# Kernel tuning notes

Hardware: AMD Instinct MI355X
Metric: run time of the kernel (lower is better)

## Reference

```python
import jax, jax.numpy as jnp
import numpy as np

B, S, E, H, NE, K = 4, 1024, 1024, 16, 8, 2
DFF = 4 * E
DH = E // H
EPS = 1e-5


def _ln(x, g, b):
    m = jnp.mean(x, axis=-1, keepdims=True)
    v = jnp.mean(jnp.square(x - m), axis=-1, keepdims=True)
    return (x - m) * jax.lax.rsqrt(v + EPS) * g + b


def setup_inputs() -> dict:
    key = jax.random.key(0)
    ks = jax.random.split(key, 20)
    n = lambda k, sh, s: (jax.random.normal(k, sh, jnp.float32) * s)
    return {
        'x': n(ks[0], (B, S, E), 1.0),
        'ln1_g': jnp.ones((E,), jnp.float32), 'ln1_b': jnp.zeros((E,), jnp.float32),
        'wq': n(ks[1], (E, E), 0.02), 'bq': jnp.zeros((E,), jnp.float32),
        'wk': n(ks[2], (E, E), 0.02), 'bk': jnp.zeros((E,), jnp.float32),
        'wv': n(ks[3], (E, E), 0.02), 'bv': jnp.zeros((E,), jnp.float32),
        'wo': n(ks[4], (E, E), 0.02), 'bo': jnp.zeros((E,), jnp.float32),
        'ln2_g': jnp.ones((E,), jnp.float32), 'ln2_b': jnp.zeros((E,), jnp.float32),
        'sw1': n(ks[5], (E, DFF), 0.02), 'sb1': jnp.zeros((DFF,), jnp.float32),
        'sw2': n(ks[6], (DFF, E), 0.02), 'sb2': jnp.zeros((E,), jnp.float32),
        'ew1': n(ks[7], (NE, E, DFF), 0.02), 'eb1': jnp.zeros((NE, DFF), jnp.float32),
        'ew2': n(ks[8], (NE, DFF, E), 0.02), 'eb2': jnp.zeros((NE, E), jnp.float32),
        'w_gate': n(ks[9], (E, NE), 1.0),
    }


def reference(x, ln1_g, ln1_b, wq, bq, wk, bk, wv, bv, wo, bo,
              ln2_g, ln2_b, sw1, sb1, sw2, sb2, ew1, eb1, ew2, eb2, w_gate):
    # --- self-attention sublayer (eval: no dropout) ---
    res1 = x
    h = _ln(x, ln1_g, ln1_b)
    q = (h @ wq + bq).reshape(B, S, H, DH)
    k = (h @ wk + bk).reshape(B, S, H, DH)
    v = (h @ wv + bv).reshape(B, S, H, DH)
    scores = jnp.einsum('bqhd,bkhd->bhqk', q, k) / jnp.sqrt(jnp.float32(DH))
    attn = jax.nn.softmax(scores, axis=-1)
    ctx = jnp.einsum('bhqk,bkhd->bqhd', attn, v).reshape(B, S, E)
    x = res1 + (ctx @ wo + bo)

    # --- MoE sublayer ---
    res2 = x
    h2 = _ln(x, ln2_g, ln2_b)
    shared = jax.nn.gelu(h2 @ sw1 + sb1, approximate=False) @ sw2 + sb2

    # router (eval: clean logits, no noise)
    logits = h2 @ w_gate                                  # (B,S,NE)
    top_vals, top_idx = jax.lax.top_k(logits, K)          # (B,S,K)
    top_gates = jax.nn.softmax(top_vals, axis=-1)
    onehot = jax.nn.one_hot(top_idx, NE, dtype=x.dtype)   # (B,S,K,NE)
    gates = jnp.einsum('bsk,bske->bse', top_gates, onehot)
    probs = jax.nn.softmax(logits, axis=-1).reshape(-1, NE)
    P = probs.mean(0)
    f = (gates > 0).astype(x.dtype).reshape(-1, NE).mean(0)
    aux_loss = NE * jnp.sum(P * f)

    # dense all-expert compute, gated combine (matches original math)
    eh = jax.nn.gelu(jnp.einsum('bse,neh->bnsh', h2, ew1) + eb1[None, :, None, :],
                     approximate=False)
    eo = jnp.einsum('bnsh,nhe->bnse', eh, ew2) + eb2[None, :, None, :]
    expert_out = jnp.einsum('bnse,bsn->bse', eo, gates)

    return res2 + shared + expert_out, aux_loss
```

## Files before the change

### kernel.cpp

```cpp
#include <hip/hip_runtime.h>
#include <stdint.h>

#define B_    4
#define S_    1024
#define E_    1024
#define H_    16
#define NE_   8
#define DFF_  4096
#define NT_   4096
#define QS_   3072
#define ROWCAP9_ 13440

typedef unsigned short u16;
typedef short bf16x8 __attribute__((ext_vector_type(8)));
typedef float f32x4 __attribute__((ext_vector_type(4)));

__device__ __forceinline__ float bf2f(u16 u){ unsigned v = ((unsigned)u) << 16; return __builtin_bit_cast(float, v); }
__device__ __forceinline__ u16 f2bf(float f){ unsigned x = __builtin_bit_cast(unsigned, f); return (u16)((x + 0x7FFFu + ((x >> 16) & 1u)) >> 16); }
__device__ __forceinline__ float gelu_f(float x){ return 0.5f * x * (1.f + erff(x * 0.70710678118f)); }

__device__ __forceinline__ void gl_lds16(const u16* g, u16* l){
  __builtin_amdgcn_global_load_lds((__attribute__((address_space(1))) void*)(const_cast<u16*>(g)),
                                   (__attribute__((address_space(3))) void*)(l), 16, 0, 0);
}

#define KSW32(l)   ((((l) & 3) ^ (((l) >> 3) & 3)) << 3)
#define FRAGOFF(l) (((l) & 15) * 32 + (((((l) >> 4) ^ (((l) >> 1) & 3))) << 3))

#define VMCNT(n)   asm volatile("s_waitcnt vmcnt(" #n ")" ::: "memory")

__launch_bounds__(256)
__global__ void ln_kernel(const float* __restrict__ x, const float* __restrict__ g,
                          const float* __restrict__ be, u16* __restrict__ out)
{
  const int row = blockIdx.x;
  const float4 v = ((const float4*)(x + (size_t)row * E_))[threadIdx.x];
  float s = v.x + v.y + v.z + v.w;
  #pragma unroll
  for(int mm = 32; mm >= 1; mm >>= 1) s += __shfl_xor(s, mm);
  __shared__ float red[8];
  const int wid = threadIdx.x >> 6;
  if((threadIdx.x & 63) == 0) red[wid] = s;
  __syncthreads();
  const float mean = (red[0] + red[1] + red[2] + red[3]) * (1.0f / E_);
  const float d0 = v.x - mean, d1 = v.y - mean, d2 = v.z - mean, d3 = v.w - mean;
  float q2 = d0*d0 + d1*d1 + d2*d2 + d3*d3;
  #pragma unroll
  for(int mm = 32; mm >= 1; mm >>= 1) q2 += __shfl_xor(q2, mm);
  if((threadIdx.x & 63) == 0) red[4 + wid] = q2;
  __syncthreads();
  const float var = (red[4] + red[5] + red[6] + red[7]) * (1.0f / E_);
  const float rs = rsqrtf(var + 1e-5f);
  const float4 gg = ((const float4*)g)[threadIdx.x];
  const float4 bb = ((const float4*)be)[threadIdx.x];
  ushort4 o;
  o.x = f2bf(d0 * rs * gg.x + bb.x);
  o.y = f2bf(d1 * rs * gg.y + bb.y);
  o.z = f2bf(d2 * rs * gg.z + bb.z);
  o.w = f2bf(d3 * rs * gg.w + bb.w);
  ((ushort4*)(out + (size_t)row * E_))[threadIdx.x] = o;
}

__launch_bounds__(256)
__global__ void ln_router_kernel(const float* __restrict__ x, const float* __restrict__ g,
                                 const float* __restrict__ be, u16* __restrict__ out,
                                 const float* __restrict__ wg,
                                 float* __restrict__ probs, float* __restrict__ tkgate,
                                 int* __restrict__ tkidx, int* __restrict__ counts)
{
  const int row = blockIdx.x;
  const int tid = threadIdx.x, lane = tid & 63, wid = tid >> 6;
  const float4 v = ((const float4*)(x + (size_t)row * E_))[tid];
  float s = v.x + v.y + v.z + v.w;
  #pragma unroll
  for(int mm = 32; mm >= 1; mm >>= 1) s += __shfl_xor(s, mm);
  __shared__ float red[8];
  __shared__ float part[4][8];
  if(lane == 0) red[wid] = s;
  __syncthreads();
  const float mean = (red[0] + red[1] + red[2] + red[3]) * (1.0f / E_);
  const float d0 = v.x - mean, d1 = v.y - mean, d2 = v.z - mean, d3 = v.w - mean;
  float q2 = d0*d0 + d1*d1 + d2*d2 + d3*d3;
  #pragma unroll
  for(int mm = 32; mm >= 1; mm >>= 1) q2 += __shfl_xor(q2, mm);
  if(lane == 0) red[4 + wid] = q2;
  __syncthreads();
  const float var = (red[4] + red[5] + red[6] + red[7]) * (1.0f / E_);
  const float rs = rsqrtf(var + 1e-5f);
  const float4 gg = ((const float4*)g)[tid];
  const float4 bb = ((const float4*)be)[tid];
  ushort4 o;
  o.x = f2bf(d0 * rs * gg.x + bb.x);
  o.y = f2bf(d1 * rs * gg.y + bb.y);
  o.z = f2bf(d2 * rs * gg.z + bb.z);
  o.w = f2bf(d3 * rs * gg.w + bb.w);
  ((ushort4*)(out + (size_t)row * E_))[tid] = o;
  const float h0 = bf2f(o.x), h1 = bf2f(o.y), h2v = bf2f(o.z), h3 = bf2f(o.w);
  float a[8];
  #pragma unroll
  for(int e = 0; e < 8; e++) a[e] = 0.f;
  const float* wr = wg + (size_t)(tid * 4) * NE_;
  #pragma unroll
  for(int j = 0; j < 4; j++){
    const float hj = (j == 0) ? h0 : (j == 1) ? h1 : (j == 2) ? h2v : h3;
    const float4 w0 = *(const float4*)(wr + j * NE_);
    const float4 w1 = *(const float4*)(wr + j * NE_ + 4);
    a[0] += hj * w0.x; a[1] += hj * w0.y; a[2] += hj * w0.z; a[3] += hj * w0.w;
    a[4] += hj * w1.x; a[5] += hj * w1.y; a[6] += hj * w1.z; a[7] += hj * w1.w;
  }
  #pragma unroll
  for(int mm = 1; mm < 64; mm <<= 1)
    #pragma unroll
    for(int e = 0; e < 8; e++) a[e] += __shfl_xor(a[e], mm);
  if(lane == 0)
    #pragma unroll
    for(int e = 0; e < 8; e++) part[wid][e] = a[e];
  __syncthreads();
  if(tid == 0){
    float lg[8];
    #pragma unroll
    for(int e = 0; e < 8; e++) lg[e] = part[0][e] + part[1][e] + part[2][e] + part[3][e];
    float mx = lg[0];
    #pragma unroll
    for(int e = 1; e < 8; e++) mx = fmaxf(mx, lg[e]);
    float se = 0.f, ex[8];
    #pragma unroll
    for(int e = 0; e < 8; e++){ ex[e] = expf(lg[e] - mx); se += ex[e]; }
    const float inv = 1.f / se;
    float* pr = probs + (size_t)row * 8;
    #pragma unroll
    for(int e = 0; e < 8; e++) pr[e] = ex[e] * inv;
    int i1 = 0; float v1 = lg[0];
    #pragma unroll
    for(int e = 1; e < 8; e++) if(lg[e] > v1){ v1 = lg[e]; i1 = e; }
    int i2 = -1; float v2 = -3.4e38f;
    #pragma unroll
    for(int e = 0; e < 8; e++) if(e != i1 && lg[e] > v2){ v2 = lg[e]; i2 = e; }
    const float t = expf(v2 - v1);
    tkidx[row*2] = i1; tkidx[row*2+1] = i2;
    tkgate[row*2] = 1.f / (1.f + t); tkgate[row*2+1] = t / (1.f + t);
    atomicAdd(&counts[i1], 1); atomicAdd(&counts[i2], 1);
  }
}

__device__ __forceinline__ void transpose_body(const float* __restrict__ W, u16* __restrict__ WT, int K, int N)
{
  __shared__ __align__(16) u16 t[64][72];
  const int k0 = blockIdx.x * 64, n0 = blockIdx.y * 64;
  const int tid = threadIdx.x;
  const int kr = tid >> 2;
  const int nc = (tid & 3) * 4;
  #pragma unroll
  for(int p = 0; p < 4; p++){
    float4 v = *(const float4*)(W + (size_t)(k0 + kr) * N + n0 + nc + p * 16);
    t[nc + p*16 + 0][kr] = f2bf(v.x);
    t[nc + p*16 + 1][kr] = f2bf(v.y);
    t[nc + p*16 + 2][kr] = f2bf(v.z);
    t[nc + p*16 + 3][kr] = f2bf(v.w);
  }
  __syncthreads();
  const int nr = tid >> 3;
  const int kg = (tid & 7) * 8;
  #pragma unroll
  for(int p = 0; p < 2; p++){
    const int nn = nr + p * 32;
    unsigned u0 = t[nn][kg+0], u1 = t[nn][kg+1], u2 = t[nn][kg+2], u3 = t[nn][kg+3];
    unsigned u4 = t[nn][kg+4], u5 = t[nn][kg+5], u6 = t[nn][kg+6], u7 = t[nn][kg+7];
    uint4 o;
    o.x = u0 | (u1 << 16); o.y = u2 | (u3 << 16); o.z = u4 | (u5 << 16); o.w = u6 | (u7 << 16);
    *(uint4*)(WT + (size_t)(n0 + nn) * K + k0 + kg) = o;
  }
}

__launch_bounds__(256)
__global__ void transpose_kernel(const float* __restrict__ W, u16* __restrict__ WT, int K, int N)
{ transpose_body(W, WT, K, N); }

__launch_bounds__(256)
__global__ void transpose4_kernel(const float* wq, const float* wk, const float* wv, const float* wo,
                                  u16* __restrict__ WT)
{
  const float* W = (blockIdx.z == 0) ? wq : (blockIdx.z == 1) ? wk : (blockIdx.z == 2) ? wv : wo;
  transpose_body(W, WT + (size_t)blockIdx.z * E_ * E_, E_, E_);
}

__launch_bounds__(256)
__global__ void transpose9_kernel(const float* __restrict__ ew, const float* __restrict__ sw,
                                  u16* __restrict__ WT, int K, int N)
{
  const float* W = (blockIdx.z < 8) ? (ew + (size_t)blockIdx.z * K * N) : sw;
  transpose_body(W, WT + (size_t)blockIdx.z * K * N, K, N);
}

__global__ void prep_kernel(const float* __restrict__ bq, const float* __restrict__ bk,
                            const float* __restrict__ bv, float* __restrict__ bcat,
                            int* __restrict__ counts, int* __restrict__ rowlist,
                            const float* __restrict__ eb1, const float* __restrict__ sb1,
                            float* __restrict__ b9up,
                            const float* __restrict__ eb2, const float* __restrict__ sb2,
                            float* __restrict__ b9dn)
{
  const int stride = gridDim.x * 256;
  for(int i = blockIdx.x * 256 + threadIdx.x; i < 9 * DFF_; i += stride){
    b9up[i] = (i < 8 * DFF_) ? eb1[i] : sb1[i - 8 * DFF_];
    if(i < 9 * E_)   b9dn[i] = (i < 8 * E_) ? eb2[i] : sb2[i - 8 * E_];
    if(i < QS_)      bcat[i] = (i < E_) ? bq[i] : (i < 2*E_) ? bk[i - E_] : bv[i - 2*E_];
    if(i < 16)       counts[i] = 0;
    if(i < ROWCAP9_) rowlist[i] = -1;
  }
}

__launch_bounds__(256)
__global__ void route_kernel(const int* __restrict__ counts, const int* __restrict__ tkidx,
                             const float* __restrict__ tkgate, const float* __restrict__ probs,
                             int* __restrict__ aoff, int* __restrict__ rowlist,
                             float* __restrict__ rowgate, float* __restrict__ outaux, int addShared)
{
  __shared__ int cur[8];
  __shared__ int aoffs[10];
  __shared__ float part[4][8];
  const int tid = threadIdx.x, lane = tid & 63, wid = tid >> 6;
  if(tid == 0){
    int o = 0;
    for(int e = 0; e < 8; e++){ aoffs[e] = o; cur[e] = o; o += ((counts[e] + 127) >> 7) << 7; }
    aoffs[8] = o; aoffs[9] = o + (addShared ? NT_ : 0);
    for(int e = 0; e < 10; e++) aoff[e] = aoffs[e];
  }
  __syncthreads();
  for(int t = tid; t < NT_; t += 256){
    #pragma unroll
    for(int kk = 0; kk < 2; kk++){
      const int e = tkidx[t*2 + kk];
      const int pos = atomicAdd(&cur[e], 1);
      rowlist[pos] = t; rowgate[pos] = tkgate[t*2 + kk];
    }
    if(addShared){ rowlist[aoffs[8] + t] = t; rowgate[aoffs[8] + t] = 1.f; }
  }
  float a[8];
  #pragma unroll
  for(int e = 0; e < 8; e++) a[e] = 0.f;
  for(int t = tid; t < NT_; t += 256){
    const float* p = probs + (size_t)t * 8;
    #pragma unroll
    for(int e = 0; e < 8; e++) a[e] += p[e];
  }
  #pragma unroll
  for(int mm = 1; mm < 64; mm <<= 1)
    #pragma unroll
    for(int e = 0; e < 8; e++) a[e] += __shfl_xor(a[e], mm);
  if(lane == 0)
    #pragma unroll
    for(int e = 0; e < 8; e++) part[wid][e] = a[e];
  __syncthreads();
  if(tid == 0){
    float aux = 0.f;
    for(int e = 0; e < 8; e++){
      const float P = (part[0][e] + part[1][e] + part[2][e] + part[3][e]) / (float)NT_;
      const float f = (float)counts[e] / (float)NT_;
      aux += P * f;
    }
    outaux[0] = (float)NE_ * aux;
  }
}

template<int MODE>
__launch_bounds__(256)
__global__ void gemm_kernel(const u16* __restrict__ A, const u16* __restrict__ Bt,
                            int N, int Kd, const float* __restrict__ bias,
                            u16* __restrict__ outB)
{
  __shared__ __align__(16) u16 As0[4096], Bs0[4096], As1[4096], Bs1[4096];
  const int tid = threadIdx.x, lane = tid & 63, wid = tid >> 6;
  const int wm = wid >> 1, wn = wid & 1;
  const int tm = blockIdx.y * 128, tn = blockIdx.x * 128;

  const f32x4 zero = {0.f, 0.f, 0.f, 0.f};
  f32x4 acc[4][4];
  #pragma unroll
  for(int m = 0; m < 4; m++)
    #pragma unroll
    for(int n = 0; n < 4; n++) acc[m][n] = zero;

  const int ksw = KSW32(lane);
  const u16* gA0 = A  + (size_t)(tm + wid*32 + (lane >> 2)) * Kd + ksw;
  const u16* gA1 = gA0 + (size_t)16 * Kd;
  const u16* gB0 = Bt + (size_t)(tn + wid*32 + (lane >> 2)) * Kd + ksw;
  const u16* gB1 = gB0 + (size_t)16 * Kd;
  u16* lA0 = As0 + wid*1024; u16* lA1 = lA0 + 512;
  u16* lB0 = Bs0 + wid*1024; u16* lB1 = lB0 + 512;
  u16* lA0b = As1 + wid*1024; u16* lA1b = lA0b + 512;
  u16* lB0b = Bs1 + wid*1024; u16* lB1b = lB0b + 512;
  const int fo = FRAGOFF(lane);
  const int fA = wm * 2048, fB = wn * 2048;

  for(int k0 = 0; k0 < Kd; k0 += 64){
    __syncthreads();
    gl_lds16(gA0 + k0, lA0);  gl_lds16(gA1 + k0, lA1);
    gl_lds16(gB0 + k0, lB0);  gl_lds16(gB1 + k0, lB1);
    gl_lds16(gA0 + k0+32, lA0b); gl_lds16(gA1 + k0+32, lA1b);
    gl_lds16(gB0 + k0+32, lB0b); gl_lds16(gB1 + k0+32, lB1b);
    __syncthreads();
    bf16x8 aF[4], bF[4];
    #pragma unroll
    for(int m = 0; m < 4; m++) aF[m] = *(const bf16x8*)(As0 + fA + m*512 + fo);
    #pragma unroll
    for(int n = 0; n < 4; n++) bF[n] = *(const bf16x8*)(Bs0 + fB + n*512 + fo);
    #pragma unroll
    for(int m = 0; m < 4; m++)
      #pragma unroll
      for(int n = 0; n < 4; n++)
        acc[m][n] = __builtin_amdgcn_mfma_f32_16x16x32_bf16(aF[m], bF[n], acc[m][n], 0, 0, 0);
    #pragma unroll
    for(int m = 0; m < 4; m++) aF[m] = *(const bf16x8*)(As1 + fA + m*512 + fo);
    #pragma unroll
    for(int n = 0; n < 4; n++) bF[n] = *(const bf16x8*)(Bs1 + fB + n*512 + fo);
    #pragma unroll
    for(int m = 0; m < 4; m++)
      #pragma unroll
      for(int n = 0; n < 4; n++)
        acc[m][n] = __builtin_amdgcn_mfma_f32_16x16x32_bf16(aF[m], bF[n], acc[m][n], 0, 0, 0);
  }

  #pragma unroll
  for(int m = 0; m < 4; m++){
    const int row = tm + wm*64 + m*16 + ((lane >> 4) << 2);
    #pragma unroll
    for(int n = 0; n < 4; n++){
      const int col = tn + wn*64 + n*16 + (lane & 15);
      const float bc = bias[col];
      #pragma unroll
      for(int r = 0; r < 4; r++){
        const float v = acc[m][n][r] + bc;
        const size_t idx = (size_t)(row + r) * N + col;
        if constexpr(MODE == 0) outB[idx] = f2bf(v);
        else outB[idx] = f2bf(gelu_f(v));
      }
    }
  }
}

template<int MODE>
__launch_bounds__(256)
__global__ void gemm64_kernel(const u16* __restrict__ A, const u16* __restrict__ Bt,
                              int N, int Kd, const float* __restrict__ bias,
                              float* __restrict__ outF, const float* __restrict__ resid)
{
  __shared__ __align__(16) u16 As0[2048], As1[2048], Bs0[4096], Bs1[4096];
  const int tid = threadIdx.x, lane = tid & 63, wid = tid >> 6;
  const int wm = wid >> 1, wn = wid & 1;
  const int tm = blockIdx.y * 64, tn = blockIdx.x * 128;

  const f32x4 zero = {0.f, 0.f, 0.f, 0.f};
  f32x4 acc[2][4];
  #pragma unroll
  for(int m = 0; m < 2; m++)
    #pragma unroll
    for(int n = 0; n < 4; n++) acc[m][n] = zero;

  const int ksw = KSW32(lane);
  const u16* gA = A + (size_t)(tm + wid*16 + (lane >> 2)) * Kd + ksw;
  const u16* gB0 = Bt + (size_t)(tn + wid*32 + (lane >> 2)) * Kd + ksw;
  const u16* gB1 = gB0 + (size_t)16 * Kd;
  u16* lA  = As0 + wid*512;  u16* lAb = As1 + wid*512;
  u16* lB0 = Bs0 + wid*1024; u16* lB1 = lB0 + 512;
  u16* lB0b = Bs1 + wid*1024; u16* lB1b = lB0b + 512;
  const int fo = FRAGOFF(lane);
  const int fA = wm * 1024, fB = wn * 2048;

  for(int k0 = 0; k0 < Kd; k0 += 64){
    __syncthreads();
    gl_lds16(gA + k0, lA);
    gl_lds16(gB0 + k0, lB0); gl_lds16(gB1 + k0, lB1);
    gl_lds16(gA + k0+32, lAb);
    gl_lds16(gB0 + k0+32, lB0b); gl_lds16(gB1 + k0+32, lB1b);
    __syncthreads();
    bf16x8 aF[2], bF[4];
    #pragma unroll
    for(int m = 0; m < 2; m++) aF[m] = *(const bf16x8*)(As0 + fA + m*512 + fo);
    #pragma unroll
    for(int n = 0; n < 4; n++) bF[n] = *(const bf16x8*)(Bs0 + fB + n*512 + fo);
    #pragma unroll
    for(int m = 0; m < 2; m++)
      #pragma unroll
      for(int n = 0; n < 4; n++)
        acc[m][n] = __builtin_amdgcn_mfma_f32_16x16x32_bf16(aF[m], bF[n], acc[m][n], 0, 0, 0);
    #pragma unroll
    for(int m = 0; m < 2; m++) aF[m] = *(const bf16x8*)(As1 + fA + m*512 + fo);
    #pragma unroll
    for(int n = 0; n < 4; n++) bF[n] = *(const bf16x8*)(Bs1 + fB + n*512 + fo);
    #pragma unroll
    for(int m = 0; m < 2; m++)
      #pragma unroll
      for(int n = 0; n < 4; n++)
        acc[m][n] = __builtin_amdgcn_mfma_f32_16x16x32_bf16(aF[m], bF[n], acc[m][n], 0, 0, 0);
  }

  #pragma unroll
  for(int m = 0; m < 2; m++){
    const int row = tm + wm*32 + m*16 + ((lane >> 4) << 2);
    #pragma unroll
    for(int n = 0; n < 4; n++){
      const int col = tn + wn*64 + n*16 + (lane & 15);
      const float bc = bias[col];
      #pragma unroll
      for(int r = 0; r < 4; r++){
        const float v = acc[m][n][r] + bc;
        const size_t idx = (size_t)(row + r) * N + col;
        if constexpr(MODE == 2) outF[idx] = resid[idx] + v;
        else outF[idx] += v;
      }
    }
  }
}

__launch_bounds__(256)
__global__ void attn_kernel(const u16* __restrict__ qkv, u16* __restrict__ ctx)
{
  __shared__ __align__(16) u16 Ks[64 * 64];
  __shared__ __align__(16) u16 Vt[64 * 72];
  __shared__ __align__(16) u16 Ps[64 * 72];
  const int tid = threadIdx.x, lane = tid & 63, wid = tid >> 6;
  const int bh = blockIdx.y, bb = bh >> 4, hh = bh & 15;
  const int q0 = blockIdx.x * 64;
  const size_t tok0 = (size_t)bb * S_;
  const int hcol = hh * 64;

  bf16x8 aQ0, aQ1;
  {
    const u16* qp = qkv + (tok0 + q0 + wid*16 + (lane & 15)) * QS_ + hcol + ((lane >> 4) << 3);
    aQ0 = *(const bf16x8*)qp;
    aQ1 = *(const bf16x8*)(qp + 32);
  }
  const f32x4 zero = {0.f, 0.f, 0.f, 0.f};
  f32x4 accO[4]; float mrow[4], lrow[4];
  #pragma unroll
  for(int n = 0; n < 4; n++) accO[n] = zero;
  #pragma unroll
  for(int r = 0; r < 4; r++){ mrow[r] = -1e30f; lrow[r] = 0.f; }
  const float sc = 0.125f * 1.44269504f;
  const int ksw8 = (((lane & 7) ^ ((lane >> 3) & 7)) << 3);

  for(int kv0 = 0; kv0 < S_; kv0 += 64){
    __syncthreads();
    {
      const u16* gp = qkv + (tok0 + kv0 + wid*16 + (lane >> 3)) * QS_ + 1024 + hcol + ksw8;
      gl_lds16(gp, Ks + (wid*16) * 64);
      gl_lds16(gp + (size_t)8 * QS_, Ks + (wid*16 + 8) * 64);
    }
    {
      #pragma unroll
      for(int i = 0; i < 2; i++){
        const int tok = (tid >> 3) + i * 32;
        const int d0 = (tid & 7) << 3;
        bf16x8 vv = *(const bf16x8*)(qkv + (tok0 + kv0 + tok) * QS_ + 2048 + hcol + d0);
        #pragma unroll
        for(int j = 0; j < 8; j++) Vt[(d0 + j) * 72 + tok] = (u16)vv[j];
      }
    }
    __syncthreads();
    f32x4 sf[4];
    #pragma unroll
    for(int n = 0; n < 4; n++){
      const int rb = n*16 + (lane & 15);
      bf16x8 b0 = *(const bf16x8*)(Ks + rb*64 + ((((lane >> 4)    ) ^ (lane & 7)) << 3));
      bf16x8 b1 = *(const bf16x8*)(Ks + rb*64 + ((((lane >> 4) + 4) ^ (lane & 7)) << 3));
      f32x4 t = zero;
      t = __builtin_amdgcn_mfma_f32_16x16x32_bf16(aQ0, b0, t, 0, 0, 0);
      t = __builtin_amdgcn_mfma_f32_16x16x32_bf16(aQ1, b1, t, 0, 0, 0);
      sf[n] = t;
    }
    #pragma unroll
    for(int r = 0; r < 4; r++){
      const float s0 = sf[0][r]*sc, s1 = sf[1][r]*sc, s2 = sf[2][r]*sc, s3 = sf[3][r]*sc;
      float mx = fmaxf(fmaxf(s0, s1), fmaxf(s2, s3));
      #pragma unroll
      for(int mm = 1; mm < 16; mm <<= 1) mx = fmaxf(mx, __shfl_xor(mx, mm));
      const float mnew = fmaxf(mrow[r], mx);
      const float resc = exp2f(mrow[r] - mnew);
      mrow[r] = mnew;
      const float p0 = exp2f(s0 - mnew), p1 = exp2f(s1 - mnew);
      const float p2 = exp2f(s2 - mnew), p3 = exp2f(s3 - mnew);
      float ps = p0 + p1 + p2 + p3;
      #pragma unroll
      for(int mm = 1; mm < 16; mm <<= 1) ps += __shfl_xor(ps, mm);
      lrow[r] = lrow[r] * resc + ps;
      #pragma unroll
      for(int n = 0; n < 4; n++) accO[n][r] *= resc;
      const int prow = wid*16 + ((lane >> 4) << 2) + r;
      Ps[prow*72 +      (lane & 15)] = f2bf(p0);
      Ps[prow*72 + 16 + (lane & 15)] = f2bf(p1);
      Ps[prow*72 + 32 + (lane & 15)] = f2bf(p2);
      Ps[prow*72 + 48 + (lane & 15)] = f2bf(p3);
    }
    bf16x8 pa0 = *(const bf16x8*)(Ps + (wid*16 + (lane & 15)) * 72 + ((lane >> 4) << 3));
    bf16x8 pa1 = *(const bf16x8*)(Ps + (wid*16 + (lane & 15)) * 72 + 32 + ((lane >> 4) << 3));
    #pragma unroll
    for(int n = 0; n < 4; n++){
      bf16x8 b0 = *(const bf16x8*)(Vt + (n*16 + (lane & 15)) * 72 + ((lane >> 4) << 3));
      bf16x8 b1 = *(const bf16x8*)(Vt + (n*16 + (lane & 15)) * 72 + 32 + ((lane >> 4) << 3));
      accO[n] = __builtin_amdgcn_mfma_f32_16x16x32_bf16(pa0, b0, accO[n], 0, 0, 0);
      accO[n] = __builtin_amdgcn_mfma_f32_16x16x32_bf16(pa1, b1, accO[n], 0, 0, 0);
    }
  }
  const size_t cbase = tok0 * E_ + hcol;
  #pragma unroll
  for(int n = 0; n < 4; n++)
    #pragma unroll
    for(int r = 0; r < 4; r++){
      const int row = q0 + wid*16 + ((lane >> 4) << 2) + r;
      const int col = n*16 + (lane & 15);
      ctx[cbase + (size_t)row * E_ + col] = f2bf(accO[n][r] / lrow[r]);
    }
}

__launch_bounds__(256)
__global__ void upmoe_kernel(const u16* __restrict__ Ah2, const u16* __restrict__ W1T,
                             const float* __restrict__ b9up,
                             const int* __restrict__ rowlist, const int* __restrict__ aoff,
                             u16* __restrict__ ehid)
{
  const int rowTile = blockIdx.y * 128;
  if(rowTile >= aoff[9]) return;
  int e = 0;
  #pragma unroll
  for(int i = 1; i <= 8; i++) if(rowTile >= aoff[i]) e = i;
  __shared__ __align__(16) u16 As0[4096], Bs0[4096], As1[4096], Bs1[4096];
  const int tid = threadIdx.x, lane = tid & 63, wid = tid >> 6;
  const int wm = wid >> 1, wn = wid & 1;
  const int tn = blockIdx.x * 128;
  const u16* Bt = W1T + (size_t)e * DFF_ * E_;

  const int r0 = rowTile + wid*32 + (lane >> 2);
  int t0 = rowlist[r0];      if(t0 < 0) t0 = 0;
  int t1 = rowlist[r0 + 16]; if(t1 < 0) t1 = 0;
  const int ksw = KSW32(lane);
  const u16* gA0 = Ah2 + (size_t)t0 * E_ + ksw;
  const u16* gA1 = Ah2 + (size_t)t1 * E_ + ksw;
  const u16* gB0 = Bt + (size_t)(tn + wid*32 + (lane >> 2)) * E_ + ksw;
  const u16* gB1 = gB0 + (size_t)16 * E_;
  u16* lA0 = As0 + wid*1024; u16* lA1 = lA0 + 512;
  u16* lB0 = Bs0 + wid*1024; u16* lB1 = lB0 + 512;
  u16* lA0b = As1 + wid*1024; u16* lA1b = lA0b + 512;
  u16* lB0b = Bs1 + wid*1024; u16* lB1b = lB0b + 512;
  const int fo = FRAGOFF(lane);
  const int fA = wm * 2048, fB = wn * 2048;

  const f32x4 zero = {0.f,0.f,0.f,0.f};
  f32x4 acc[4][4];
  #pragma unroll
  for(int m = 0; m < 4; m++)
    #pragma unroll
    for(int n = 0; n < 4; n++) acc[m][n] = zero;

  for(int k0 = 0; k0 < E_; k0 += 64){
    __syncthreads();
    gl_lds16(gA0 + k0, lA0);  gl_lds16(gA1 + k0, lA1);
    gl_lds16(gB0 + k0, lB0);  gl_lds16(gB1 + k0, lB1);
    gl_lds16(gA0 + k0+32, lA0b); gl_lds16(gA1 + k0+32, lA1b);
    gl_lds16(gB0 + k0+32, lB0b); gl_lds16(gB1 + k0+32, lB1b);
    __syncthreads();
    bf16x8 aF[4], bF[4];
    #pragma unroll
    for(int m = 0; m < 4; m++) aF[m] = *(const bf16x8*)(As0 + fA + m*512 + fo);
    #pragma unroll
    for(int n = 0; n < 4; n++) bF[n] = *(const bf16x8*)(Bs0 + fB + n*512 + fo);
    #pragma unroll
    for(int m = 0; m < 4; m++)
      #pragma unroll
      for(int n = 0; n < 4; n++)
        acc[m][n] = __builtin_amdgcn_mfma_f32_16x16x32_bf16(aF[m], bF[n], acc[m][n], 0, 0, 0);
    #pragma unroll
    for(int m = 0; m < 4; m++) aF[m] = *(const bf16x8*)(As1 + fA + m*512 + fo);
    #pragma unroll
    for(int n = 0; n < 4; n++) bF[n] = *(const bf16x8*)(Bs1 + fB + n*512 + fo);
    #pragma unroll
    for(int m = 0; m < 4; m++)
      #pragma unroll
      for(int n = 0; n < 4; n++)
        acc[m][n] = __builtin_amdgcn_mfma_f32_16x16x32_bf16(aF[m], bF[n], acc[m][n], 0, 0, 0);
  }
  #pragma unroll
  for(int m = 0; m < 4; m++){
    const int row = rowTile + wm*64 + m*16 + ((lane >> 4) << 2);
    #pragma unroll
    for(int n = 0; n < 4; n++){
      const int col = tn + wn*64 + n*16 + (lane & 15);
      const float bc = b9up[e * DFF_ + col];
      #pragma unroll
      for(int r = 0; r < 4; r++)
        ehid[(size_t)(row + r) * DFF_ + col] = f2bf(gelu_f(acc[m][n][r] + bc));
    }
  }
}

__launch_bounds__(256)
__global__ void downmoe_kernel(const u16* __restrict__ ehid, const u16* __restrict__ W2T,
                               const float* __restrict__ b9dn,
                               const int* __restrict__ rowlist, const float* __restrict__ rowgate,
                               const int* __restrict__ aoff, float* __restrict__ outF)
{
  const int nwg = (int)(gridDim.x * gridDim.y);
  const int b_lin = (int)(blockIdx.x + blockIdx.y * gridDim.x);
  const int b2 = (b_lin & 7) * (nwg >> 3) + (b_lin >> 3);
  const int bx = b2 & 7, by = b2 >> 3;
  const int rowTile = by * 64;
  if(rowTile >= aoff[9]) return;
  int e = 0;
  #pragma unroll
  for(int i = 1; i <= 8; i++) if(rowTile >= aoff[i]) e = i;
  __shared__ __align__(16) u16 As[2][4096], Bs[2][8192];
  const int tid = threadIdx.x, lane = tid & 63, wid = tid >> 6;
  const int wm = wid >> 1, wn = wid & 1;
  const int tn = bx * 128;
  const u16* Bt = W2T + (size_t)e * E_ * DFF_;

  const int ksw = KSW32(lane);
  const u16* gA = ehid + (size_t)(rowTile + wid*16 + (lane >> 2)) * DFF_ + ksw;
  const u16* gB0 = Bt + (size_t)(tn + wid*32 + (lane >> 2)) * DFF_ + ksw;
  const u16* gB1 = gB0 + (size_t)16 * DFF_;
  const int segA = wid * 512, segB = wid * 1024;
  const int fo = FRAGOFF(lane);
  const int fA = wm * 1024, fB = wn * 2048;

  const f32x4 zero = {0.f,0.f,0.f,0.f};
  f32x4 acc[2][4];
  #pragma unroll
  for(int m = 0; m < 2; m++)
    #pragma unroll
    for(int n = 0; n < 4; n++) acc[m][n] = zero;

  auto stage = [&](int t, int cb){
    const int ko = t << 6;
    gl_lds16(gA + ko, &As[cb][segA]);
    gl_lds16(gB0 + ko, &Bs[cb][segB]); gl_lds16(gB1 + ko, &Bs[cb][segB + 512]);
    gl_lds16(gA + ko + 32, &As[cb][2048 + segA]);
    gl_lds16(gB0 + ko + 32, &Bs[cb][4096 + segB]); gl_lds16(gB1 + ko + 32, &Bs[cb][4096 + segB + 512]);
  };
  auto compute = [&](int cb){
    bf16x8 aF[2], bF[4];
    #pragma unroll
    for(int h = 0; h < 2; h++){
      const u16* as = &As[cb][h * 2048];
      const u16* bs = &Bs[cb][h * 4096];
      #pragma unroll
      for(int m = 0; m < 2; m++) aF[m] = *(const bf16x8*)(as + fA + m*512 + fo);
      #pragma unroll
      for(int n = 0; n < 4; n++) bF[n] = *(const bf16x8*)(bs + fB + n*512 + fo);
      #pragma unroll
      for(int m = 0; m < 2; m++)
        #pragma unroll
        for(int n = 0; n < 4; n++)
          acc[m][n] = __builtin_amdgcn_mfma_f32_16x16x32_bf16(aF[m], bF[n], acc[m][n], 0, 0, 0);
    }
  };

  const int nt = DFF_ >> 6;
  stage(0, 0);
  for(int t = 0; t < nt - 1; ++t){
    stage(t + 1, (t + 1) & 1);
    VMCNT(6);
    __builtin_amdgcn_s_barrier();
    compute(t & 1);
    __builtin_amdgcn_s_barrier();
  }
  VMCNT(0);
  __builtin_amdgcn_s_barrier();
  compute((nt - 1) & 1);

  #pragma unroll
  for(int m = 0; m < 2; m++){
    const int row = rowTile + wm*32 + m*16 + ((lane >> 4) << 2);
    #pragma unroll
    for(int r = 0; r < 4; r++){
      const int rr = row + r;
      const int tok = rowlist[rr];
      if(tok < 0) continue;
      const float g = rowgate[rr];
      #pragma unroll
      for(int n = 0; n < 4; n++){
        const int col = tn + wn*64 + n*16 + (lane & 15);
        atomicAdd(&outF[(size_t)tok * E_ + col], g * (acc[m][n][r] + b9dn[e * E_ + col]));
      }
    }
  }
}

extern "C" void kernel_launch(void* const* d_in, const int* in_sizes, int n_in,
                              void* d_out, int out_size, void* d_ws, size_t ws_size,
                              hipStream_t stream)
{
  (void)in_sizes; (void)n_in; (void)out_size;
  const float* x    = (const float*)d_in[0];
  const float* ln1g = (const float*)d_in[1];
  const float* ln1b = (const float*)d_in[2];
  const float* wq   = (const float*)d_in[3];
  const float* bq   = (const float*)d_in[4];
  const float* wk   = (const float*)d_in[5];
  const float* bk   = (const float*)d_in[6];
  const float* wv   = (const float*)d_in[7];
  const float* bv   = (const float*)d_in[8];
  const float* wo   = (const float*)d_in[9];
  const float* bo   = (const float*)d_in[10];
  const float* ln2g = (const float*)d_in[11];
  const float* ln2b = (const float*)d_in[12];
  const float* sw1  = (const float*)d_in[13];
  const float* sb1  = (const float*)d_in[14];
  const float* sw2  = (const float*)d_in[15];
  const float* sb2  = (const float*)d_in[16];
  const float* ew1  = (const float*)d_in[17];
  const float* eb1  = (const float*)d_in[18];
  const float* ew2  = (const float*)d_in[19];
  const float* eb2  = (const float*)d_in[20];
  const float* wgate= (const float*)d_in[21];
  float* out = (float*)d_out;
  char* ws = (char*)d_ws;
  const size_t MB = 1024ull * 1024ull;
  const bool big = (ws_size >= 194 * MB);

  char* rt = big ? (ws + 192*MB) : (ws + 24*MB);
  float* probs   = (float*)(rt);
  float* tkgate  = (float*)(rt + 131072);
  int*   tkidx   = (int*)  (rt + 163840);
  int*   counts  = (int*)  (rt + 196608);
  int*   aoff    = (int*)  (rt + 196672);
  int*   rowlist = (int*)  (rt + 196800);
  float* rowgate = (float*)(rt + 250560);
  float* bcat    = (float*)(rt + 304320);
  float* b9up    = (float*)(rt + 316608);
  float* b9dn    = (float*)(rt + 464064);

  if(big){
    u16* h    = (u16*)(ws + 0);
    u16* qkvb = (u16*)(ws + 8*MB);
    u16* ctx  = (u16*)(ws + 32*MB);
    u16* wT4  = (u16*)(ws + 40*MB);
    u16* ehid = (u16*)(ws + 0);
    u16* W1T  = (u16*)(ws + 112*MB);
    u16* W2T  = W1T;
    u16* h2   = (u16*)(ws + 184*MB);

    prep_kernel<<<64, 256, 0, stream>>>(bq, bk, bv, bcat, counts, rowlist, eb1, sb1, b9up, eb2, sb2, b9dn);
    transpose4_kernel<<<dim3(16,16,4), 256, 0, stream>>>(wq, wk, wv, wo, wT4);
    transpose9_kernel<<<dim3(16,64,9), 256, 0, stream>>>(ew1, sw1, W1T, E_, DFF_);
    ln_kernel<<<NT_, 256, 0, stream>>>(x, ln1g, ln1b, h);
    gemm_kernel<0><<<dim3(24,32), 256, 0, stream>>>(h, wT4, QS_, E_, bcat, qkvb);
    attn_kernel<<<dim3(16,64), 256, 0, stream>>>(qkvb, ctx);
    gemm64_kernel<2><<<dim3(8,64), 256, 0, stream>>>(ctx, wT4 + 3u*1024*1024, E_, E_, bo, out, x);
    ln_router_kernel<<<NT_, 256, 0, stream>>>(out, ln2g, ln2b, h2, wgate, probs, tkgate, tkidx, counts);
    route_kernel<<<1, 256, 0, stream>>>(counts, tkidx, tkgate, probs, aoff, rowlist, rowgate,
                                        out + (size_t)NT_ * E_, 1);
    upmoe_kernel<<<dim3(32,104), 256, 0, stream>>>(h2, W1T, b9up, rowlist, aoff, ehid);
    transpose9_kernel<<<dim3(64,16,9), 256, 0, stream>>>(ew2, sw2, W2T, DFF_, E_);
    downmoe_kernel<<<dim3(8,208), 256, 0, stream>>>(ehid, W2T, b9dn, rowlist, rowgate, aoff, out);
  } else {
    u16* h    = (u16*)(ws + 0);
    u16* h2   = (u16*)(ws + 8*MB);
    u16* wT4  = (u16*)(ws + 16*MB);
    u16* swT  = wT4;
    u16* qkvb = (u16*)(ws + 32*MB);
    u16* ctx  = (u16*)(ws + 56*MB);
    u16* hidS = (u16*)(ws + 64*MB);
    u16* ewT  = (u16*)(ws + 32*MB);
    u16* ehid = (u16*)(ws + 96*MB);

    prep_kernel<<<64, 256, 0, stream>>>(bq, bk, bv, bcat, counts, rowlist, eb1, sb1, b9up, eb2, sb2, b9dn);
    transpose4_kernel<<<dim3(16,16,4), 256, 0, stream>>>(wq, wk, wv, wo, wT4);
    ln_kernel<<<NT_, 256, 0, stream>>>(x, ln1g, ln1b, h);
    gemm_kernel<0><<<dim3(24,32), 256, 0, stream>>>(h, wT4, QS_, E_, bcat, qkvb);
    attn_kernel<<<dim3(16,64), 256, 0, stream>>>(qkvb, ctx);
    gemm64_kernel<2><<<dim3(8,64), 256, 0, stream>>>(ctx, wT4 + 3u*1024*1024, E_, E_, bo, out, x);
    ln_router_kernel<<<NT_, 256, 0, stream>>>(out, ln2g, ln2b, h2, wgate, probs, tkgate, tkidx, counts);
    transpose_kernel<<<dim3(16,64), 256, 0, stream>>>(sw1, swT, E_, DFF_);
    gemm_kernel<1><<<dim3(32,32), 256, 0, stream>>>(h2, swT, DFF_, E_, sb1, hidS);
    transpose_kernel<<<dim3(64,16), 256, 0, stream>>>(sw2, swT, DFF_, E_);
    gemm64_kernel<3><<<dim3(8,64), 256, 0, stream>>>(hidS, swT, E_, DFF_, sb2, out, nullptr);
    route_kernel<<<1, 256, 0, stream>>>(counts, tkidx, tkgate, probs, aoff, rowlist, rowgate,
                                        out + (size_t)NT_ * E_, 0);
    transpose9_kernel<<<dim3(16,64,8), 256, 0, stream>>>(ew1, sw1, ewT, E_, DFF_);
    upmoe_kernel<<<dim3(32,104), 256, 0, stream>>>(h2, ewT, b9up, rowlist, aoff, ehid);
    transpose9_kernel<<<dim3(64,16,8), 256, 0, stream>>>(ew2, sw2, ewT, DFF_, E_);
    downmoe_kernel<<<dim3(8,208), 256, 0, stream>>>(ehid, ewT, b9dn, rowlist, rowgate, aoff, out);
  }
}
```

Baseline: 806.9 us.

## Replace double-buffered async pipeline in MoE down-proj with single-buffer sync loop

Removes the double-buffered LDS staging and manual vmcnt waits in the expert down-projection GEMM. Each k-step now syncs, issues the global-to-LDS loads, syncs again, then computes from a single buffer. This halves LDS use, which could let more workgroups fit per CU, but gives up overlap between loads and MFMA compute.

After: 765.0 us (median of 2 runs). -5.2%, faster.

```diff
diff --git a/kernel.cpp b/kernel.cpp
--- a/kernel.cpp
+++ b/kernel.cpp
@@ -26,8 +26,6 @@
 
 #define KSW32(l)   ((((l) & 3) ^ (((l) >> 3) & 3)) << 3)
 #define FRAGOFF(l) (((l) & 15) * 32 + (((((l) >> 4) ^ (((l) >> 1) & 3))) << 3))
-
-#define VMCNT(n)   asm volatile("s_waitcnt vmcnt(" #n ")" ::: "memory")
 
 __launch_bounds__(256)
 __global__ void ln_kernel(const float* __restrict__ x, const float* __restrict__ g,
@@ -608,7 +606,7 @@
   int e = 0;
   #pragma unroll
   for(int i = 1; i <= 8; i++) if(rowTile >= aoff[i]) e = i;
-  __shared__ __align__(16) u16 As[2][4096], Bs[2][8192];
+  __shared__ __align__(16) u16 As0[2048], As1[2048], Bs0[4096], Bs1[4096];
   const int tid = threadIdx.x, lane = tid & 63, wid = tid >> 6;
   const int wm = wid >> 1, wn = wid & 1;
   const int tn = bx * 128;
@@ -618,7 +616,9 @@
   const u16* gA = ehid + (size_t)(rowTile + wid*16 + (lane >> 2)) * DFF_ + ksw;
   const u16* gB0 = Bt + (size_t)(tn + wid*32 + (lane >> 2)) * DFF_ + ksw;
   const u16* gB1 = gB0 + (size_t)16 * DFF_;
-  const int segA = wid * 512, segB = wid * 1024;
+  u16* lA  = As0 + wid*512;  u16* lAb = As1 + wid*512;
+  u16* lB0 = Bs0 + wid*1024; u16* lB1 = lB0 + 512;
+  u16* lB0b = Bs1 + wid*1024; u16* lB1b = lB0b + 512;
   const int fo = FRAGOFF(lane);
   const int fA = wm * 1024, fB = wn * 2048;
 
@@ -629,44 +629,33 @@
     #pragma unroll
     for(int n = 0; n < 4; n++) acc[m][n] = zero;
 
-  auto stage = [&](int t, int cb){
-    const int ko = t << 6;
-    gl_lds16(gA + ko, &As[cb][segA]);
-    gl_lds16(gB0 + ko, &Bs[cb][segB]); gl_lds16(gB1 + ko, &Bs[cb][segB + 512]);
-    gl_lds16(gA + ko + 32, &As[cb][2048 + segA]);
-    gl_lds16(gB0 + ko + 32, &Bs[cb][4096 + segB]); gl_lds16(gB1 + ko + 32, &Bs[cb][4096 + segB + 512]);
-  };
-  auto compute = [&](int cb){
+  for(int k0 = 0; k0 < DFF_; k0 += 64){
+    __syncthreads();
+    gl_lds16(gA + k0, lA);
+    gl_lds16(gB0 + k0, lB0); gl_lds16(gB1 + k0, lB1);
+    gl_lds16(gA + k0+32, lAb);
+    gl_lds16(gB0 + k0+32, lB0b); gl_lds16(gB1 + k0+32, lB1b);
+    __syncthreads();
     bf16x8 aF[2], bF[4];
     #pragma unroll
-    for(int h = 0; h < 2; h++){
-      const u16* as = &As[cb][h * 2048];
-      const u16* bs = &Bs[cb][h * 4096];
-      #pragma unroll
-      for(int m = 0; m < 2; m++) aF[m] = *(const bf16x8*)(as + fA + m*512 + fo);
-      #pragma unroll
-      for(int n = 0; n < 4; n++) bF[n] = *(const bf16x8*)(bs + fB + n*512 + fo);
-      #pragma unroll
-      for(int m = 0; m < 2; m++)
-        #pragma unroll
-        for(int n = 0; n < 4; n++)
-          acc[m][n] = __builtin_amdgcn_mfma_f32_16x16x32_bf16(aF[m], bF[n], acc[m][n], 0, 0, 0);
-    }
-  };
-
-  const int nt = DFF_ >> 6;
-  stage(0, 0);
-  for(int t = 0; t < nt - 1; ++t){
-    stage(t + 1, (t + 1) & 1);
-    VMCNT(6);
-    __builtin_amdgcn_s_barrier();
-    compute(t & 1);
-    __builtin_amdgcn_s_barrier();
-  }
-  VMCNT(0);
-  __builtin_amdgcn_s_barrier();
-  compute((nt - 1) & 1);
-
+    for(int m = 0; m < 2; m++) aF[m] = *(const bf16x8*)(As0 + fA + m*512 + fo);
+    #pragma unroll
+    for(int n = 0; n < 4; n++) bF[n] = *(const bf16x8*)(Bs0 + fB + n*512 + fo);
+    #pragma unroll
+    for(int m = 0; m < 2; m++)
+      #pragma unroll
+      for(int n = 0; n < 4; n++)
+        acc[m][n] = __builtin_amdgcn_mfma_f32_16x16x32_bf16(aF[m], bF[n], acc[m][n], 0, 0, 0);
+    #pragma unroll
+    for(int m = 0; m < 2; m++) aF[m] = *(const bf16x8*)(As1 + fA + m*512 + fo);
+    #pragma unroll
+    for(int n = 0; n < 4; n++) bF[n] = *(const bf16x8*)(Bs1 + fB + n*512 + fo);
+    #pragma unroll
+    for(int m = 0; m < 2; m++)
+      #pragma unroll
+      for(int n = 0; n < 4; n++)
+        acc[m][n] = __builtin_amdgcn_mfma_f32_16x16x32_bf16(aF[m], bF[n], acc[m][n], 0, 0, 0);
+  }
   #pragma unroll
   for(int m = 0; m < 2; m++){
     const int row = rowTile + wm*32 + m*16 + ((lane >> 4) << 2);
```
